# Optimization experiments

Hardware: AMD Instinct MI355X
Metric: run time of the kernel (lower is better)

Reference implementation:

```python
import jax, jax.numpy as jnp
import numpy as np

NUM_HEADS = 8
HEAD_DIM = 64  # output_size
HIDDEN = 512
N_NODES = 4096


def setup_inputs() -> dict:
    key = jax.random.key(0)
    ks = jax.random.split(key, 9)
    s = 0.02
    return {
        "x": jax.random.normal(ks[0], (N_NODES, HIDDEN), dtype=jnp.float32),
        "Wq_w": jax.random.normal(ks[1], (HIDDEN, NUM_HEADS * HEAD_DIM), dtype=jnp.float32) * s,
        "Wq_b": jax.random.normal(ks[2], (NUM_HEADS * HEAD_DIM,), dtype=jnp.float32) * s,
        "Wk_w": jax.random.normal(ks[3], (HIDDEN, NUM_HEADS * HEAD_DIM), dtype=jnp.float32) * s,
        "Wk_b": jax.random.normal(ks[4], (NUM_HEADS * HEAD_DIM,), dtype=jnp.float32) * s,
        "Wv_w": jax.random.normal(ks[5], (HIDDEN, NUM_HEADS * HEAD_DIM), dtype=jnp.float32) * s,
        "Wv_b": jax.random.normal(ks[6], (NUM_HEADS * HEAD_DIM,), dtype=jnp.float32) * s,
        "Wo_w": jax.random.normal(ks[7], (NUM_HEADS * HEAD_DIM, HEAD_DIM), dtype=jnp.float32) * s,
        "Wo_b": jax.random.normal(ks[8], (HEAD_DIM,), dtype=jnp.float32) * s,
    }


def reference(x, Wq_w, Wq_b, Wk_w, Wk_b, Wv_w, Wv_b, Wo_w, Wo_b):
    N = x.shape[0]
    H, d = NUM_HEADS, HEAD_DIM
    # Projections: [N, H*d] -> [H, N, d]
    q = (x @ Wq_w + Wq_b).reshape(N, H, d).transpose(1, 0, 2)
    k = (x @ Wk_w + Wk_b).reshape(N, H, d).transpose(1, 0, 2)
    v = (x @ Wv_w + Wv_b).reshape(N, H, d).transpose(1, 0, 2)
    # Scaled dot-product attention per head: [H, N, N]
    scores = jnp.einsum('hnd,hmd->hnm', q, k) / jnp.sqrt(jnp.float32(d))
    attention_weights = jax.nn.softmax(scores, axis=-1)
    attended = jnp.einsum('hnm,hmd->hnd', attention_weights, v)  # [H, N, d]
    attended = attended.transpose(1, 0, 2).reshape(N, H * d)
    output = attended @ Wo_w + Wo_b  # [N, d]
    return output, attention_weights
```

## Files before the change

kernel.cpp:

```cpp
#include <hip/hip_runtime.h>

#define NN 4096
#define HID 512
#define NH 8
#define HD 64

typedef __attribute__((ext_vector_type(8))) short short8;
typedef __attribute__((ext_vector_type(4))) float f32x4;

__device__ __forceinline__ ushort f2bf(float f) {
    unsigned u = __float_as_uint(f);
    return (ushort)((u + 0x7FFFu + ((u >> 16) & 1u)) >> 16);
}

__device__ __forceinline__ void gld16(const void* g, void* l) {
    __builtin_amdgcn_global_load_lds(
        (const __attribute__((address_space(1))) void*)g,
        (__attribute__((address_space(3))) void*)l, 16, 0, 0);
}

__global__ __launch_bounds__(256) void qkv_kernel(
    const float* __restrict__ x,
    const float* __restrict__ Wq, const float* __restrict__ bq,
    const float* __restrict__ Wk, const float* __restrict__ bk,
    const float* __restrict__ Wv, const float* __restrict__ bv,
    ushort* __restrict__ Qb, char* __restrict__ Kbs, char* __restrict__ Vts)
{
    const int mat = blockIdx.z;
    const float* W = (mat == 0) ? Wq : ((mat == 1) ? Wk : Wv);
    const float* b = (mat == 0) ? bq : ((mat == 1) ? bk : bv);

    const int row0 = blockIdx.y * 128;
    const int col0 = blockIdx.x * 64;
    const int tid = threadIdx.x;
    const int tx = tid & 15, ty = tid >> 4;

    __shared__ float xs[32][132];
    __shared__ float wt[32][68];
    __shared__ __align__(16) ushort vts[64][136];

    float acc[8][4];
#pragma unroll
    for (int i = 0; i < 8; ++i)
#pragma unroll
        for (int j = 0; j < 4; ++j) acc[i][j] = 0.f;

    for (int kc = 0; kc < HID; kc += 32) {
#pragma unroll
        for (int it = 0; it < 4; ++it) {
            int f = it * 256 + tid;
            int i = f >> 3, k4 = f & 7;
            float4 v = *(const float4*)(x + (size_t)(row0 + i) * HID + kc + k4 * 4);
            xs[k4 * 4 + 0][i] = v.x; xs[k4 * 4 + 1][i] = v.y;
            xs[k4 * 4 + 2][i] = v.z; xs[k4 * 4 + 3][i] = v.w;
        }
#pragma unroll
        for (int it = 0; it < 2; ++it) {
            int f = it * 256 + tid;
            int k = f >> 4, c4 = f & 15;
            float4 v = *(const float4*)(W + (size_t)(kc + k) * HID + col0 + c4 * 4);
            *(float4*)&wt[k][c4 * 4] = v;
        }
        __syncthreads();
        for (int k = 0; k < 32; ++k) {
            float a0[8], b0[4];
            *(float4*)&a0[0] = *(const float4*)&xs[k][ty * 4];
            *(float4*)&a0[4] = *(const float4*)&xs[k][64 + ty * 4];
            *(float4*)&b0[0] = *(const float4*)&wt[k][tx * 4];
#pragma unroll
            for (int i = 0; i < 8; ++i)
#pragma unroll
                for (int j = 0; j < 4; ++j)
                    acc[i][j] = fmaf(a0[i], b0[j], acc[i][j]);
        }
        __syncthreads();
    }

    const int head = col0 >> 6;
    if (mat == 0) {
#pragma unroll
        for (int bi = 0; bi < 2; ++bi)
#pragma unroll
            for (int ii = 0; ii < 4; ++ii) {
                int r = row0 + bi * 64 + ty * 4 + ii;
                ushort4 u;
                u.x = f2bf(acc[bi * 4 + ii][0] + b[col0 + tx * 4 + 0]);
                u.y = f2bf(acc[bi * 4 + ii][1] + b[col0 + tx * 4 + 1]);
                u.z = f2bf(acc[bi * 4 + ii][2] + b[col0 + tx * 4 + 2]);
                u.w = f2bf(acc[bi * 4 + ii][3] + b[col0 + tx * 4 + 3]);
                *(ushort4*)(Qb + ((size_t)head * NN + r) * HD + tx * 4) = u;
            }
    } else if (mat == 1) {
#pragma unroll
        for (int bi = 0; bi < 2; ++bi)
#pragma unroll
            for (int ii = 0; ii < 4; ++ii) {
                int r = row0 + bi * 64 + ty * 4 + ii;
                ushort4 u;
                u.x = f2bf(acc[bi * 4 + ii][0] + b[col0 + tx * 4 + 0]);
                u.y = f2bf(acc[bi * 4 + ii][1] + b[col0 + tx * 4 + 1]);
                u.z = f2bf(acc[bi * 4 + ii][2] + b[col0 + tx * 4 + 2]);
                u.w = f2bf(acc[bi * 4 + ii][3] + b[col0 + tx * 4 + 3]);
                int bc = (tx * 8) ^ ((r & 7) << 4);
                *(ushort4*)(Kbs + ((size_t)head * NN + r) * 128 + bc) = u;
            }
    } else {
#pragma unroll
        for (int bi = 0; bi < 2; ++bi)
#pragma unroll
            for (int ii = 0; ii < 4; ++ii) {
                int rl = bi * 64 + ty * 4 + ii;
#pragma unroll
                for (int j = 0; j < 4; ++j) {
                    int cl = tx * 4 + j;
                    vts[cl][rl] = f2bf(acc[bi * 4 + ii][j] + b[col0 + cl]);
                }
            }
        __syncthreads();
        int cl = tid >> 2, q = tid & 3;
        int dsw = (cl & 7) << 4;
        char* dstrow = Vts + (size_t)(col0 + cl) * NN * 2;
        int colb0 = (row0 + q * 32) * 2;
#pragma unroll
        for (int k8 = 0; k8 < 4; ++k8)
            *(uint4*)(dstrow + ((colb0 + k8 * 16) ^ dsw)) =
                *(const uint4*)(&vts[cl][q * 32 + k8 * 8]);
    }
}

__global__ __launch_bounds__(512, 4) void attn_kernel(
    const ushort* __restrict__ Qb, const char* __restrict__ Kbs,
    const char* __restrict__ Vts,
    float* __restrict__ wout, float* __restrict__ att)
{
    const int h = blockIdx.x & 7;
    const int row0 = ((blockIdx.x >> 3) + (blockIdx.y << 3)) * 64;
    const int tid = threadIdx.x;
    const int w = tid >> 6, lane = tid & 63;
    const int g = lane >> 4, li = lane & 15;
    const int rgrp = w >> 1, khalf = w & 1;
    const int qr = row0 + rgrp * 16;

    const ushort* Qh = Qb + (size_t)h * NN * HD;
    const char* Kh = Kbs + (size_t)h * NN * 128;
    const char* Vh = Vts + (size_t)h * HD * NN * 2;
    float* WH = wout + ((size_t)h << 24);

    __shared__ __align__(16) char smem[81920];
    char* kbuf0 = smem;
    char* kbuf1 = smem + 16384;
    char* vbuf0 = smem + 32768;
    char* vbuf1 = smem + 49152;
    char* pbuf  = smem + 65536;
    float* zpart = (float*)(smem + 65536);
    float* attstage = (float*)(smem + 65536);

    const short8 qa0 = *(const short8*)(Qh + (size_t)(qr + li) * HD + g * 8);
    const short8 qa1 = *(const short8*)(Qh + (size_t)(qr + li) * HD + 32 + g * 8);
    const int sw = (li & 7) << 4;

    const int kl0 = w * 16 + (lane >> 3);
    const int kbase0 = (kl0 & 63) + ((kl0 >= 64) ? 2048 : 0);
    const int kl1 = kl0 + 8;
    const int kbase1 = (kl1 & 63) + ((kl1 >= 64) ? 2048 : 0);
    const size_t koff0 = (size_t)kbase0 * 128 + (lane & 7) * 16;
    const size_t koff1 = (size_t)kbase1 * 128 + (lane & 7) * 16;
    const int vd0 = w * 8 + (lane >> 4);
    const int vd1 = vd0 + 4;
    const size_t voff0 = (size_t)vd0 * 8192 + ((lane >> 3) & 1) * 4096 + (lane & 7) * 16;
    const size_t voff1 = (size_t)vd1 * 8192 + ((lane >> 3) & 1) * 4096 + (lane & 7) * 16;
    const int ldst = w * 2048 + lane * 16;

    float zsum = 0.f;
    {
        char* c0 = kbuf0; char* c1 = kbuf1; char* c2 = vbuf0;
        gld16(Kh + koff0, c0 + ldst);
        gld16(Kh + koff1, c0 + ldst + 1024);
        gld16(Kh + 8192 + koff0, c1 + ldst);
        gld16(Kh + 8192 + koff1, c1 + ldst + 1024);
        asm volatile("" ::: "memory");
        for (int t = 0; t < 32; ++t) {
            if (t < 31) { asm volatile("s_waitcnt vmcnt(2)" ::: "memory"); }
            else        { asm volatile("s_waitcnt vmcnt(0)" ::: "memory"); }
            __builtin_amdgcn_s_barrier();
            if (t + 2 < 32) {
                gld16(Kh + (size_t)(t + 2) * 8192 + koff0, c2 + ldst);
                gld16(Kh + (size_t)(t + 2) * 8192 + koff1, c2 + ldst + 1024);
            }
            asm volatile("" ::: "memory");
#pragma unroll
            for (int jt = 0; jt < 4; ++jt) {
                const char* rp = c0 + (khalf * 64 + jt * 16 + li) * 128;
                short8 kb0 = *(const short8*)(rp + ((g * 16) ^ sw));
                short8 kb1 = *(const short8*)(rp + ((64 + g * 16) ^ sw));
                f32x4 acc = {0.f, 0.f, 0.f, 0.f};
                acc = __builtin_amdgcn_mfma_f32_16x16x32_bf16(kb0, qa0, acc, 0, 0, 0);
                acc = __builtin_amdgcn_mfma_f32_16x16x32_bf16(kb1, qa1, acc, 0, 0, 0);
#pragma unroll
                for (int r = 0; r < 4; ++r) zsum += __expf(acc[r] * 0.125f);
            }
            char* tmp = c0; c0 = c1; c1 = c2; c2 = tmp;
        }
    }
    zsum += __shfl_xor(zsum, 16);
    zsum += __shfl_xor(zsum, 32);
    if (lane < 16) zpart[w * 16 + li] = zsum;
    __syncthreads();
    const float iz = 1.0f / (zpart[(rgrp * 2) * 16 + li] + zpart[(rgrp * 2 + 1) * 16 + li]);
    __syncthreads();

    f32x4 pv[4];
#pragma unroll
    for (int dt = 0; dt < 4; ++dt) pv[dt] = (f32x4){0.f, 0.f, 0.f, 0.f};
    char* myp = pbuf + w * 2048;

    {
        char* kc = kbuf0; char* kn = kbuf1;
        char* vc = vbuf0; char* vn = vbuf1;
        gld16(Kh + koff0, kc + ldst);
        gld16(Kh + koff1, kc + ldst + 1024);
        gld16(Vh + voff0, vc + ldst);
        gld16(Vh + voff1, vc + ldst + 1024);
        asm volatile("" ::: "memory");
        for (int t = 0; t < 32; ++t) {
            if (t == 0) { asm volatile("s_waitcnt vmcnt(0)" ::: "memory"); }
            else        { asm volatile("s_waitcnt vmcnt(4)" ::: "memory"); }
            __builtin_amdgcn_s_barrier();
            if (t + 1 < 32) {
                gld16(Kh + (size_t)(t + 1) * 8192 + koff0, kn + ldst);
                gld16(Kh + (size_t)(t + 1) * 8192 + koff1, kn + ldst + 1024);
                gld16(Vh + (size_t)(t + 1) * 128 + voff0, vn + ldst);
                gld16(Vh + (size_t)(t + 1) * 128 + voff1, vn + ldst + 1024);
            }
            asm volatile("" ::: "memory");
#pragma unroll
            for (int jt = 0; jt < 4; ++jt) {
                const char* rp = kc + (khalf * 64 + jt * 16 + li) * 128;
                short8 kb0 = *(const short8*)(rp + ((g * 16) ^ sw));
                short8 kb1 = *(const short8*)(rp + ((64 + g * 16) ^ sw));
                f32x4 acc = {0.f, 0.f, 0.f, 0.f};
                acc = __builtin_amdgcn_mfma_f32_16x16x32_bf16(kb0, qa0, acc, 0, 0, 0);
                acc = __builtin_amdgcn_mfma_f32_16x16x32_bf16(kb1, qa1, acc, 0, 0, 0);
                f32x4 ev;
#pragma unroll
                for (int r = 0; r < 4; ++r) ev[r] = __expf(acc[r] * 0.125f) * iz;
                *(f32x4*)(WH + (size_t)(qr + li) * NN + khalf * 2048 + t * 64 + jt * 16 + g * 4) = ev;
                uint pk0 = (uint)f2bf(ev[0]) | ((uint)f2bf(ev[1]) << 16);
                uint pk1 = (uint)f2bf(ev[2]) | ((uint)f2bf(ev[3]) << 16);
                int boff = (li * 128 + jt * 32 + g * 8) ^ sw;
                *(uint2*)(myp + boff) = make_uint2(pk0, pk1);
            }
#pragma unroll
            for (int kb2 = 0; kb2 < 2; ++kb2) {
                int rbp = (li * 128 + kb2 * 64 + g * 16) ^ sw;
                short8 pa = *(const short8*)(myp + rbp);
#pragma unroll
                for (int dt = 0; dt < 4; ++dt) {
                    const char* vrp = vc + (dt * 16 + li) * 256 + khalf * 128;
                    short8 vbf = *(const short8*)(vrp + ((kb2 * 64 + g * 16) ^ sw));
                    pv[dt] = __builtin_amdgcn_mfma_f32_16x16x32_bf16(pa, vbf, pv[dt], 0, 0, 0);
                }
            }
            char* tmp = kc; kc = kn; kn = tmp;
            tmp = vc; vc = vn; vn = tmp;
        }
    }

    __syncthreads();
    if (khalf == 1) {
#pragma unroll
        for (int dt = 0; dt < 4; ++dt)
#pragma unroll
            for (int r = 0; r < 4; ++r)
                attstage[(rgrp * 16 + g * 4 + r) * 64 + dt * 16 + li] = pv[dt][r];
    }
    __syncthreads();
    if (khalf == 0) {
#pragma unroll
        for (int dt = 0; dt < 4; ++dt)
#pragma unroll
            for (int r = 0; r < 4; ++r) {
                float v = pv[dt][r] + attstage[(rgrp * 16 + g * 4 + r) * 64 + dt * 16 + li];
                att[(size_t)(qr + g * 4 + r) * HID + h * HD + dt * 16 + li] = v;
            }
    }
}

__global__ __launch_bounds__(256) void out_kernel(
    const float* __restrict__ att, const float* __restrict__ Wo,
    const float* __restrict__ bo, float* __restrict__ outp)
{
    const int row0 = blockIdx.x * 16;
    const int tid = threadIdx.x;
    const int tx = tid & 15, ty = tid >> 4;

    __shared__ float as_[64][20];
    __shared__ float ws2[64][68];

    float acc[4] = {0.f, 0.f, 0.f, 0.f};

    for (int kc = 0; kc < HID; kc += 64) {
        {
            int i = tid >> 4, k4 = tid & 15;
            float4 v = *(const float4*)(att + (size_t)(row0 + i) * HID + kc + k4 * 4);
            as_[k4 * 4 + 0][i] = v.x; as_[k4 * 4 + 1][i] = v.y;
            as_[k4 * 4 + 2][i] = v.z; as_[k4 * 4 + 3][i] = v.w;
        }
#pragma unroll
        for (int it = 0; it < 4; ++it) {
            int f = it * 256 + tid;
            int k = f >> 4, c4 = f & 15;
            float4 v = *(const float4*)(Wo + (size_t)(kc + k) * HD + c4 * 4);
            *(float4*)&ws2[k][c4 * 4] = v;
        }
        __syncthreads();
        for (int k = 0; k < 64; ++k) {
            float a = as_[k][ty];
            float4 b0 = *(const float4*)&ws2[k][tx * 4];
            acc[0] = fmaf(a, b0.x, acc[0]);
            acc[1] = fmaf(a, b0.y, acc[1]);
            acc[2] = fmaf(a, b0.z, acc[2]);
            acc[3] = fmaf(a, b0.w, acc[3]);
        }
        __syncthreads();
    }

    float4 v;
    v.x = acc[0] + bo[tx * 4 + 0];
    v.y = acc[1] + bo[tx * 4 + 1];
    v.z = acc[2] + bo[tx * 4 + 2];
    v.w = acc[3] + bo[tx * 4 + 3];
    *(float4*)(outp + (size_t)(row0 + ty) * HD + tx * 4) = v;
}

extern "C" void kernel_launch(void* const* d_in, const int* in_sizes, int n_in,
                              void* d_out, int out_size, void* d_ws, size_t ws_size,
                              hipStream_t stream) {
    const float* x  = (const float*)d_in[0];
    const float* Wq = (const float*)d_in[1];
    const float* bq = (const float*)d_in[2];
    const float* Wk = (const float*)d_in[3];
    const float* bk = (const float*)d_in[4];
    const float* Wv = (const float*)d_in[5];
    const float* bv = (const float*)d_in[6];
    const float* Wo = (const float*)d_in[7];
    const float* bo = (const float*)d_in[8];

    float* out  = (float*)d_out;
    float* wout = out + (size_t)NN * HD;

    char* wsb = (char*)d_ws;
    ushort* Qb  = (ushort*)wsb;
    char*   Kbs = wsb + 4u * 1024u * 1024u;
    char*   Vts = wsb + 8u * 1024u * 1024u;
    float*  att = (float*)(wsb + 12u * 1024u * 1024u);

    hipLaunchKernelGGL(qkv_kernel, dim3(8, 32, 3), dim3(256), 0, stream,
                       x, Wq, bq, Wk, bk, Wv, bv, Qb, Kbs, Vts);
    hipLaunchKernelGGL(attn_kernel, dim3(64, NH), dim3(512), 0, stream,
                       Qb, Kbs, Vts, wout, att);
    hipLaunchKernelGGL(out_kernel, dim3(256), dim3(256), 0, stream,
                       att, Wo, bo, out);
}
```

Before: 278.3 us.

## Compute QKV projection with split-bf16 MFMA instead of FP32 FMA

```diff
diff --git a/kernel.cpp b/kernel.cpp
--- a/kernel.cpp
+++ b/kernel.cpp
@@ -12,6 +12,9 @@
     unsigned u = __float_as_uint(f);
     return (ushort)((u + 0x7FFFu + ((u >> 16) & 1u)) >> 16);
 }
+__device__ __forceinline__ float bf2f(ushort h) {
+    return __uint_as_float((unsigned)h << 16);
+}
 
 __device__ __forceinline__ void gld16(const void* g, void* l) {
     __builtin_amdgcn_global_load_lds(
@@ -19,112 +22,157 @@
         (__attribute__((address_space(3))) void*)l, 16, 0, 0);
 }
 
-__global__ __launch_bounds__(256) void qkv_kernel(
-    const float* __restrict__ x,
-    const float* __restrict__ Wq, const float* __restrict__ bq,
-    const float* __restrict__ Wk, const float* __restrict__ bk,
-    const float* __restrict__ Wv, const float* __restrict__ bv,
+__global__ __launch_bounds__(256) void cvt_x_kernel(
+    const float* __restrict__ x, ushort* __restrict__ xh, ushort* __restrict__ xl)
+{
+    int i = (blockIdx.x * 256 + threadIdx.x) * 8;
+    float4 v0 = *(const float4*)(x + i);
+    float4 v1 = *(const float4*)(x + i + 4);
+    float v[8] = {v0.x, v0.y, v0.z, v0.w, v1.x, v1.y, v1.z, v1.w};
+    ushort h[8], l[8];
+#pragma unroll
+    for (int j = 0; j < 8; ++j) {
+        h[j] = f2bf(v[j]);
+        l[j] = f2bf(v[j] - bf2f(h[j]));
+    }
+    ushort4 u;
+    u.x = h[0]; u.y = h[1]; u.z = h[2]; u.w = h[3]; *(ushort4*)(xh + i) = u;
+    u.x = h[4]; u.y = h[5]; u.z = h[6]; u.w = h[7]; *(ushort4*)(xh + i + 4) = u;
+    u.x = l[0]; u.y = l[1]; u.z = l[2]; u.w = l[3]; *(ushort4*)(xl + i) = u;
+    u.x = l[4]; u.y = l[5]; u.z = l[6]; u.w = l[7]; *(ushort4*)(xl + i + 4) = u;
+}
+
+__global__ __launch_bounds__(256) void cvt_w_kernel(
+    const float* __restrict__ Wq, const float* __restrict__ Wk,
+    const float* __restrict__ Wv,
+    ushort* __restrict__ Wph, ushort* __restrict__ Wpl)
+{
+    const int mat = blockIdx.z;
+    const float* W = (mat == 0) ? Wq : ((mat == 1) ? Wk : Wv);
+    const int col = blockIdx.x * 256 + threadIdx.x;
+    const int kcb = blockIdx.y;
+    ushort* dh = Wph + (size_t)mat * 262144 + kcb * 16384 + col * 32;
+    ushort* dl = Wpl + (size_t)mat * 262144 + kcb * 16384 + col * 32;
+#pragma unroll
+    for (int k4 = 0; k4 < 8; ++k4) {
+        ushort4 uh, ul;
+#pragma unroll
+        for (int j = 0; j < 4; ++j) {
+            float v = W[(size_t)(kcb * 32 + k4 * 4 + j) * HID + col];
+            ushort h = f2bf(v);
+            (&uh.x)[j] = h;
+            (&ul.x)[j] = f2bf(v - bf2f(h));
+        }
+        *(ushort4*)(dh + k4 * 4) = uh;
+        *(ushort4*)(dl + k4 * 4) = ul;
+    }
+}
+
+__global__ __launch_bounds__(256) void qkv_mfma_kernel(
+    const ushort* __restrict__ xh, const ushort* __restrict__ xl,
+    const ushort* __restrict__ Wph, const ushort* __restrict__ Wpl,
+    const float* __restrict__ bq, const float* __restrict__ bk,
+    const float* __restrict__ bv,
     ushort* __restrict__ Qb, char* __restrict__ Kbs, char* __restrict__ Vts)
 {
     const int mat = blockIdx.z;
-    const float* W = (mat == 0) ? Wq : ((mat == 1) ? Wk : Wv);
-    const float* b = (mat == 0) ? bq : ((mat == 1) ? bk : bv);
-
     const int row0 = blockIdx.y * 128;
     const int col0 = blockIdx.x * 64;
     const int tid = threadIdx.x;
-    const int tx = tid & 15, ty = tid >> 4;
-
-    __shared__ float xs[32][132];
-    __shared__ float wt[32][68];
-    __shared__ __align__(16) ushort vts[64][136];
-
-    float acc[8][4];
-#pragma unroll
-    for (int i = 0; i < 8; ++i)
-#pragma unroll
-        for (int j = 0; j < 4; ++j) acc[i][j] = 0.f;
-
-    for (int kc = 0; kc < HID; kc += 32) {
-#pragma unroll
-        for (int it = 0; it < 4; ++it) {
-            int f = it * 256 + tid;
-            int i = f >> 3, k4 = f & 7;
-            float4 v = *(const float4*)(x + (size_t)(row0 + i) * HID + kc + k4 * 4);
-            xs[k4 * 4 + 0][i] = v.x; xs[k4 * 4 + 1][i] = v.y;
-            xs[k4 * 4 + 2][i] = v.z; xs[k4 * 4 + 3][i] = v.w;
-        }
-#pragma unroll
-        for (int it = 0; it < 2; ++it) {
-            int f = it * 256 + tid;
-            int k = f >> 4, c4 = f & 15;
-            float4 v = *(const float4*)(W + (size_t)(kc + k) * HID + col0 + c4 * 4);
-            *(float4*)&wt[k][c4 * 4] = v;
-        }
+    const int w = tid >> 6, lane = tid & 63, g = lane >> 4, li = lane & 15;
+    const ushort* Bh = Wph + (size_t)mat * 262144;
+    const ushort* Bl = Wpl + (size_t)mat * 262144;
+    const float* bias = (mat == 0) ? bq : ((mat == 1) ? bk : bv);
+
+    __shared__ __align__(16) char smem[18432];
+
+    f32x4 acc[2][4];
+#pragma unroll
+    for (int sb = 0; sb < 2; ++sb)
+#pragma unroll
+        for (int cf = 0; cf < 4; ++cf) acc[sb][cf] = (f32x4){0.f, 0.f, 0.f, 0.f};
+
+    const ushort* xr0h = xh + (size_t)(row0 + w * 32 + li) * HID;
+    const ushort* xr1h = xr0h + 16 * HID;
+    const ushort* xr0l = xl + (size_t)(row0 + w * 32 + li) * HID;
+    const ushort* xr1l = xr0l + 16 * HID;
+
+#pragma unroll 2
+    for (int kcb = 0; kcb < 16; ++kcb) {
+        const int ko = kcb * 32 + g * 8;
+        short8 a0h = *(const short8*)(xr0h + ko);
+        short8 a1h = *(const short8*)(xr1h + ko);
+        short8 a0l = *(const short8*)(xr0l + ko);
+        short8 a1l = *(const short8*)(xr1l + ko);
+        const ushort* bbh = Bh + kcb * 16384 + (col0 + li) * 32 + g * 8;
+        const ushort* bbl = Bl + kcb * 16384 + (col0 + li) * 32 + g * 8;
+#pragma unroll
+        for (int cf = 0; cf < 4; ++cf) {
+            short8 bhf = *(const short8*)(bbh + cf * 512);
+            short8 blf = *(const short8*)(bbl + cf * 512);
+            acc[0][cf] = __builtin_amdgcn_mfma_f32_16x16x32_bf16(a0l, bhf, acc[0][cf], 0, 0, 0);
+            acc[0][cf] = __builtin_amdgcn_mfma_f32_16x16x32_bf16(a0h, blf, acc[0][cf], 0, 0, 0);
+            acc[0][cf] = __builtin_amdgcn_mfma_f32_16x16x32_bf16(a0h, bhf, acc[0][cf], 0, 0, 0);
+            acc[1][cf] = __builtin_amdgcn_mfma_f32_16x16x32_bf16(a1l, bhf, acc[1][cf], 0, 0, 0);
+            acc[1][cf] = __builtin_amdgcn_mfma_f32_16x16x32_bf16(a1h, blf, acc[1][cf], 0, 0, 0);
+            acc[1][cf] = __builtin_amdgcn_mfma_f32_16x16x32_bf16(a1h, bhf, acc[1][cf], 0, 0, 0);
+        }
+    }
+
+    float bv_f[4];
+#pragma unroll
+    for (int cf = 0; cf < 4; ++cf) bv_f[cf] = bias[col0 + cf * 16 + li];
+
+    const int head = col0 >> 6;
+    if (mat < 2) {
+        ushort* st = (ushort*)smem;
+#pragma unroll
+        for (int sb = 0; sb < 2; ++sb)
+#pragma unroll
+            for (int cf = 0; cf < 4; ++cf)
+#pragma unroll
+                for (int r = 0; r < 4; ++r)
+                    st[(w * 32 + sb * 16 + g * 4 + r) * 72 + cf * 16 + li] =
+                        f2bf(acc[sb][cf][r] + bv_f[cf]);
         __syncthreads();
-        for (int k = 0; k < 32; ++k) {
-            float a0[8], b0[4];
-            *(float4*)&a0[0] = *(const float4*)&xs[k][ty * 4];
-            *(float4*)&a0[4] = *(const float4*)&xs[k][64 + ty * 4];
-            *(float4*)&b0[0] = *(const float4*)&wt[k][tx * 4];
-#pragma unroll
-            for (int i = 0; i < 8; ++i)
-#pragma unroll
-                for (int j = 0; j < 4; ++j)
-                    acc[i][j] = fmaf(a0[i], b0[j], acc[i][j]);
-        }
-        __syncthreads();
-    }
-
-    const int head = col0 >> 6;
-    if (mat == 0) {
-#pragma unroll
-        for (int bi = 0; bi < 2; ++bi)
-#pragma unroll
-            for (int ii = 0; ii < 4; ++ii) {
-                int r = row0 + bi * 64 + ty * 4 + ii;
-                ushort4 u;
-                u.x = f2bf(acc[bi * 4 + ii][0] + b[col0 + tx * 4 + 0]);
-                u.y = f2bf(acc[bi * 4 + ii][1] + b[col0 + tx * 4 + 1]);
-                u.z = f2bf(acc[bi * 4 + ii][2] + b[col0 + tx * 4 + 2]);
-                u.w = f2bf(acc[bi * 4 + ii][3] + b[col0 + tx * 4 + 3]);
-                *(ushort4*)(Qb + ((size_t)head * NN + r) * HD + tx * 4) = u;
-            }
-    } else if (mat == 1) {
-#pragma unroll
-        for (int bi = 0; bi < 2; ++bi)
-#pragma unroll
-            for (int ii = 0; ii < 4; ++ii) {
-                int r = row0 + bi * 64 + ty * 4 + ii;
-                ushort4 u;
-                u.x = f2bf(acc[bi * 4 + ii][0] + b[col0 + tx * 4 + 0]);
-                u.y = f2bf(acc[bi * 4 + ii][1] + b[col0 + tx * 4 + 1]);
-                u.z = f2bf(acc[bi * 4 + ii][2] + b[col0 + tx * 4 + 2]);
-                u.w = f2bf(acc[bi * 4 + ii][3] + b[col0 + tx * 4 + 3]);
-                int bc = (tx * 8) ^ ((r & 7) << 4);
-                *(ushort4*)(Kbs + ((size_t)head * NN + r) * 128 + bc) = u;
-            }
+        int row = tid >> 1, hf = tid & 1;
+        const ushort* src = st + row * 72 + hf * 32;
+        if (mat == 0) {
+            ushort* dst = Qb + ((size_t)head * NN + row0 + row) * HD + hf * 32;
+#pragma unroll
+            for (int c = 0; c < 4; ++c)
+                *(uint4*)(dst + c * 8) = *(const uint4*)(src + c * 8);
+        } else {
+            char* dst = Kbs + ((size_t)head * NN + row0 + row) * 128;
+#pragma unroll
+            for (int j8 = 0; j8 < 4; ++j8) {
+                int j = hf * 4 + j8;
+                *(uint4*)(dst + ((j * 16) ^ ((row & 7) << 4))) =
+                    *(const uint4*)(st + row * 72 + j * 8);
+            }
+        }
     } else {
-#pragma unroll
-        for (int bi = 0; bi < 2; ++bi)
-#pragma unroll
-            for (int ii = 0; ii < 4; ++ii) {
-                int rl = bi * 64 + ty * 4 + ii;
-#pragma unroll
-                for (int j = 0; j < 4; ++j) {
-                    int cl = tx * 4 + j;
-                    vts[cl][rl] = f2bf(acc[bi * 4 + ii][j] + b[col0 + cl]);
-                }
+        ushort* vst = (ushort*)smem;
+#pragma unroll
+        for (int sb = 0; sb < 2; ++sb)
+#pragma unroll
+            for (int cf = 0; cf < 4; ++cf) {
+                ushort4 pk;
+                pk.x = f2bf(acc[sb][cf][0] + bv_f[cf]);
+                pk.y = f2bf(acc[sb][cf][1] + bv_f[cf]);
+                pk.z = f2bf(acc[sb][cf][2] + bv_f[cf]);
+                pk.w = f2bf(acc[sb][cf][3] + bv_f[cf]);
+                *(ushort4*)(vst + (cf * 16 + li) * 136 + w * 32 + sb * 16 + g * 4) = pk;
             }
         __syncthreads();
         int cl = tid >> 2, q = tid & 3;
         int dsw = (cl & 7) << 4;
-        char* dstrow = Vts + (size_t)(col0 + cl) * NN * 2;
+        char* dstrow = Vts + (size_t)(col0 + cl) * (NN * 2);
         int colb0 = (row0 + q * 32) * 2;
 #pragma unroll
         for (int k8 = 0; k8 < 4; ++k8)
             *(uint4*)(dstrow + ((colb0 + k8 * 16) ^ dsw)) =
-                *(const uint4*)(&vts[cl][q * 32 + k8 * 8]);
+                *(const uint4*)(vst + cl * 136 + q * 32 + k8 * 8);
     }
 }
 
@@ -354,9 +402,16 @@
     char*   Kbs = wsb + 4u * 1024u * 1024u;
     char*   Vts = wsb + 8u * 1024u * 1024u;
     float*  att = (float*)(wsb + 12u * 1024u * 1024u);
-
-    hipLaunchKernelGGL(qkv_kernel, dim3(8, 32, 3), dim3(256), 0, stream,
-                       x, Wq, bq, Wk, bk, Wv, bv, Qb, Kbs, Vts);
+    ushort* xh  = (ushort*)(wsb + 20u * 1024u * 1024u);
+    ushort* xl  = (ushort*)(wsb + 24u * 1024u * 1024u);
+    ushort* Wph = (ushort*)(wsb + 28u * 1024u * 1024u);
+    ushort* Wpl = (ushort*)(wsb + 30u * 1024u * 1024u);
+
+    hipLaunchKernelGGL(cvt_x_kernel, dim3(1024), dim3(256), 0, stream, x, xh, xl);
+    hipLaunchKernelGGL(cvt_w_kernel, dim3(2, 16, 3), dim3(256), 0, stream,
+                       Wq, Wk, Wv, Wph, Wpl);
+    hipLaunchKernelGGL(qkv_mfma_kernel, dim3(8, 32, 3), dim3(256), 0, stream,
+                       xh, xl, Wph, Wpl, bq, bk, bv, Qb, Kbs, Vts);
     hipLaunchKernelGGL(attn_kernel, dim3(64, NH), dim3(512), 0, stream,
                        Qb, Kbs, Vts, wout, att);
     hipLaunchKernelGGL(out_kernel, dim3(256), dim3(256), 0, stream,
```

New measurement: 246.3 us. 1.13x faster.
